# Optimization experiments

Hardware: AMD Instinct MI355X
Metric: run time of the kernel (lower is better)

## Reference

```python
import jax, jax.numpy as jnp
import numpy as np

B, N_P, N_S = 64, 50, 200
N_NODES = N_P * N_S          # 10000 nodes per graph (jobs x ops)
N_CAND = N_S + 1             # 201 candidates
INPUT_DIM, HIDDEN = 3, 64
NODE_DIM = 2 * HIDDEN        # h_nodes feature dim (=> actor in = 6*HIDDEN)
POOL_DIM = 4 * HIDDEN        # h_pooled dim (mean || max pooling)
H_ACTOR, H_CRITIC = 256, 256


def setup_inputs() -> dict:
    key = jax.random.key(0)
    ks = jax.random.split(key, 16)
    p = lambda k, sh: jax.random.normal(k, sh, jnp.float32) * 0.02
    x = jax.random.normal(ks[0], (B, N_NODES, INPUT_DIM), jnp.float32)
    candidate = jax.random.randint(ks[1], (B, N_CAND), 0, N_NODES)
    mask = jax.random.randint(ks[2], (B, N_CAND), 0, 2) > 0
    mask = mask.at[:, 0].set(True)  # guarantee at least one valid action per row
    return {
        "x": x, "candidate": candidate, "mask": mask,
        "fe_w1": p(ks[3], (INPUT_DIM, HIDDEN)), "fe_b1": jnp.zeros((HIDDEN,), jnp.float32),
        "fe_w2": p(ks[4], (HIDDEN, NODE_DIM)), "fe_b2": jnp.zeros((NODE_DIM,), jnp.float32),
        "a_w1": p(ks[5], (NODE_DIM + POOL_DIM, H_ACTOR)), "a_b1": jnp.zeros((H_ACTOR,), jnp.float32),
        "a_w2": p(ks[6], (H_ACTOR, H_ACTOR)), "a_b2": jnp.zeros((H_ACTOR,), jnp.float32),
        "a_w3": p(ks[7], (H_ACTOR, 1)), "a_b3": jnp.zeros((1,), jnp.float32),
        "c_w1": p(ks[8], (POOL_DIM, H_CRITIC)), "c_b1": jnp.zeros((H_CRITIC,), jnp.float32),
        "c_w2": p(ks[9], (H_CRITIC, H_CRITIC)), "c_b2": jnp.zeros((H_CRITIC,), jnp.float32),
        "c_w3": p(ks[10], (H_CRITIC, 1)), "c_b3": jnp.zeros((1,), jnp.float32),
    }


def _actor_critic(x, candidate, mask,
                  fe_w1, fe_b1, fe_w2, fe_b2,
                  a_w1, a_b1, a_w2, a_b2, a_w3, a_b3,
                  c_w1, c_b1, c_w2, c_b2, c_w3, c_b3):
    # --- feature_extract: per-node MLP embedding, graph-level pooling ---
    h = jax.nn.relu(jnp.einsum('bni,ih->bnh', x, fe_w1) + fe_b1)
    h_nodes = jax.nn.relu(jnp.einsum('bnh,hd->bnd', h, fe_w2) + fe_b2)   # [B, N, 2H]
    h_pooled = jnp.concatenate([h_nodes.mean(axis=1), h_nodes.max(axis=1)], axis=-1)  # [B, 4H]

    # --- gather candidate node features (torch.gather over node axis) ---
    cand_feat = jnp.take_along_axis(h_nodes, candidate[:, :, None], axis=1)  # [B, C, 2H]

    # --- concat broadcast pooled feature ---
    pooled_rep = jnp.broadcast_to(h_pooled[:, None, :], (cand_feat.shape[0], cand_feat.shape[1], h_pooled.shape[-1]))
    concat_fea = jnp.concatenate([cand_feat, pooled_rep], axis=-1)  # [B, C, 6H]

    # --- actor MLP (tanh hidden layers, linear out) ---
    a = jnp.tanh(concat_fea @ a_w1 + a_b1)
    a = jnp.tanh(a @ a_w2 + a_b2)
    scores = a @ a_w3 + a_b3                                    # [B, C, 1]

    # --- mask with -inf, softmax over candidate axis ---
    scores = jnp.where(mask[:, :, None], scores, -jnp.inf)
    pi = jax.nn.softmax(scores, axis=1)                          # [B, C, 1]

    # --- critic MLP on pooled feature ---
    c = jnp.tanh(h_pooled @ c_w1 + c_b1)
    c = jnp.tanh(c @ c_w2 + c_b2)
    v = c @ c_w3 + c_b3                                          # [B, 1]
    return pi, v


def reference(x, candidate, mask,
              fe_w1, fe_b1, fe_w2, fe_b2,
              a_w1, a_b1, a_w2, a_b2, a_w3, a_b3,
              c_w1, c_b1, c_w2, c_b2, c_w3, c_b3):
    return _actor_critic(x, candidate, mask,
                         fe_w1, fe_b1, fe_w2, fe_b2,
                         a_w1, a_b1, a_w2, a_b2, a_w3, a_b3,
                         c_w1, c_b1, c_w2, c_b2, c_w3, c_b3)
```

## Files before the change

### kernel.cpp

```cpp
#include <hip/hip_runtime.h>

#define NN 10000
#define NCAND 201
#define NB 64

typedef __attribute__((ext_vector_type(8))) short short8;
typedef __attribute__((ext_vector_type(4))) float f32x4;

__device__ __forceinline__ float bf2f(unsigned short u) {
  return __uint_as_float(((unsigned int)u) << 16);
}
__device__ __forceinline__ unsigned short f2bf(float f) {
  unsigned int u = __float_as_uint(f);
  u += 0x7FFFu + ((u >> 16) & 1u);
  return (unsigned short)(u >> 16);
}
__device__ __forceinline__ float fast_tanh(float x) {
  return 1.0f - 2.0f / (__expf(2.0f * x) + 1.0f);
}
__device__ __forceinline__ float gld(const void* p, long i, int f) {
  return f ? ((const float*)p)[i] : bf2f(((const unsigned short*)p)[i]);
}

__global__ __launch_bounds__(256)
void prep_kernel(const void* x, const void* w1, const void* b1, const void* w2,
                 const void* b2, const void* aw1, const void* ab1, const void* aw2,
                 const void* ab2, const void* aw3, const void* ab3,
                 const void* cw1, const void* cb1, const void* cw2, const void* cb2,
                 const void* cw3, const void* cb3,
                 const unsigned int* mask_w, const unsigned int* cand_w,
                 int* F, float* zero_base, int* scnt,
                 unsigned short* __restrict__ w2t, unsigned short* __restrict__ aw1t,
                 unsigned short* __restrict__ aw2t,
                 unsigned short* __restrict__ cw1t, unsigned short* __restrict__ cw2t) {
  const int t = threadIdx.x;
  const int j = blockIdx.x;

  if (j < 384) {
    __shared__ int cnts[5];
    if (t < 5) cnts[t] = 0;
    __syncthreads();
    const void* aps[5] = {w2, aw1, aw2, cw1, cw2};
#pragma unroll
    for (int a = 0; a < 5; ++a) {
      const unsigned short* p = (const unsigned short*)aps[a];
      if ((p[t] & 0x7F80u) >= 0x4300u) atomicAdd(&cnts[a], 1);
    }
    __syncthreads();
    const int Fw2 = cnts[0] > 32, Faw1 = cnts[1] > 32, Faw2 = cnts[2] > 32;
    const int Fcw1 = cnts[3] > 32, Fcw2 = cnts[4] > 32;
    int i = j * 256 + t;
    if (i < 128 * 64) { int n = i >> 6, k = i & 63; w2t[i] = f2bf(gld(w2, k * 128 + n, Fw2)); }
    if (i < 256 * 384) { int n = i / 384, k = i % 384; aw1t[i] = f2bf(gld(aw1, k * 256 + n, Faw1)); }
    if (i < 256 * 256) {
      int n = i >> 8, k = i & 255;
      aw2t[i] = f2bf(gld(aw2, k * 256 + n, Faw2));
      cw1t[i] = f2bf(gld(cw1, k * 256 + n, Fcw1));
      cw2t[i] = f2bf(gld(cw2, k * 256 + n, Fcw2));
    }
    return;
  }

  __shared__ int sh[3];
  if (t < 3) sh[t] = 0;
  __syncthreads();

  if (j < 401) {
    const void* ptrs[17] = {x, w1, b1, w2, b2, aw1, ab1, aw2, ab2, aw3, ab3,
                            cw1, cb1, cw2, cb2, cw3, cb3};
    const int sizes[17] = {1920000, 192, 64, 8192, 128, 98304, 256, 65536, 256,
                           256, 1, 65536, 256, 65536, 256, 256, 1};
    int a = j - 384;
    const unsigned short* p = (const unsigned short*)ptrs[a];
    int K = min(sizes[a], 2048);
    int c = 0;
    for (int i = t; i < K; i += 256)
      if ((p[i] & 0x7F80u) >= 0x4300u) c++;
    if (c) atomicAdd(&sh[0], c);
    __syncthreads();
    if (t == 0) F[a] = (sh[0] > (K >> 3)) ? 1 : 0;
  } else if (j == 401) {
    int flo = 0, fhi = 0, fgt = 0;
    for (int i = t; i < 3216; i += 256) {
      unsigned int w = mask_w[i];
      if ((w & 0xFFFFu) == 0x3F80u) flo = 1;
      if ((w >> 16) == 0x3F80u) fhi = 1;
      if (w > 1u) fgt = 1;
    }
    if (flo) sh[0] = 1;
    if (fhi) sh[1] = 1;
    if (fgt) sh[2] = 1;
    __syncthreads();
    if (t == 0) F[17] = sh[0] ? 2 : (sh[1] ? 3 : (sh[2] ? 1 : 0));
  } else if (j == 402) {
    int co = 0;
    for (int i = t; i < 1024; i += 256)
      if ((i & 1) && cand_w[i] != 0u) co = 1;
    if (co) sh[0] = 1;
    if (t < 64) scnt[t] = 0;
    __syncthreads();
    if (t == 0) F[18] = sh[0] ? 0 : 1;
  } else {
    zero_base[(j - 403) * 256 + t] = 0.f;
  }
}

__global__ __launch_bounds__(256, 4)
void fp_actorA_kernel(const void* __restrict__ x, const int* __restrict__ cand,
                      const void* __restrict__ w1, const void* __restrict__ b1,
                      const unsigned short* __restrict__ w2t,
                      const void* __restrict__ b2,
                      const int* __restrict__ F,
                      float* __restrict__ psum, float* __restrict__ pmax,
                      unsigned short* __restrict__ cfw) {
  __shared__ __align__(16) unsigned short pool[128 * 72];
  __shared__ float w1f[3 * 64];
  __shared__ float b1f[64];
  __shared__ float b2f[128];

  const int t = threadIdx.x;
  const int lane = t & 63;
  const int wv = t >> 6;
  const int F0 = F[0], F1 = F[1], F2 = F[2], F4 = F[4];

  if (blockIdx.x < 1024) {
    unsigned short* h1s = pool;
    const int b = blockIdx.x >> 4;
    const int s = blockIdx.x & 15;

    if (t < 192) w1f[t] = gld(w1, t, F1);
    if (t < 64) b1f[t] = gld(b1, t, F2);
    if (t < 128) b2f[t] = gld(b2, t, F4);

    short8 bfr[2][2];
#pragma unroll
    for (int nl = 0; nl < 2; ++nl)
#pragma unroll
      for (int ks = 0; ks < 2; ++ks) {
        int col = wv * 32 + nl * 16 + (lane & 15);
        bfr[nl][ks] = *(const short8*)(w2t + col * 64 + ((lane >> 4) * 8) + ks * 32);
      }
    __syncthreads();

    float csum[2] = {0.f, 0.f};
    float cmax[2] = {0.f, 0.f};
    const int m = t & 127;
    const int kg = t >> 7;

    float x0 = 0.f, x1 = 0.f, x2 = 0.f;
    if (s < 79) {
      int nb = s * 128;
      if (m < min(128, NN - nb)) {
        long xo = ((long)b * NN + nb + m) * 3;
        x0 = gld(x, xo, F0); x1 = gld(x, xo + 1, F0); x2 = gld(x, xo + 2, F0);
      }
    }

    for (int c = s; c < 79; c += 16) {
      int nb = c * 128;
      int cnt = (nb + 128 <= NN) ? 128 : (NN - nb);
      if (m < cnt) {
#pragma unroll
        for (int blk = 0; blk < 4; ++blk) {
          short8 v;
#pragma unroll
          for (int i = 0; i < 8; ++i) {
            int k = kg * 32 + blk * 8 + i;
            float vv = x0 * w1f[k] + x1 * w1f[64 + k] + x2 * w1f[128 + k] + b1f[k];
            v[i] = (short)f2bf(fmaxf(vv, 0.f));
          }
          *(short8*)(h1s + m * 72 + kg * 32 + blk * 8) = v;
        }
      }
      {
        int cn = c + 16;
        float nx0 = 0.f, nx1 = 0.f, nx2 = 0.f;
        if (cn < 79) {
          int nbn = cn * 128;
          if (m < min(128, NN - nbn)) {
            long xo = ((long)b * NN + nbn + m) * 3;
            nx0 = gld(x, xo, F0); nx1 = gld(x, xo + 1, F0); nx2 = gld(x, xo + 2, F0);
          }
        }
        __syncthreads();
        x0 = nx0; x1 = nx1; x2 = nx2;
      }
#pragma unroll
      for (int mt = 0; mt < 8; ++mt) {
        const unsigned short* ap = h1s + (mt * 16 + (lane & 15)) * 72 + ((lane >> 4) * 8);
        short8 af0 = *(const short8*)(ap);
        short8 af1 = *(const short8*)(ap + 32);
#pragma unroll
        for (int nl = 0; nl < 2; ++nl) {
          f32x4 acc = {0.f, 0.f, 0.f, 0.f};
          acc = __builtin_amdgcn_mfma_f32_16x16x32_bf16(af0, bfr[nl][0], acc, 0, 0, 0);
          acc = __builtin_amdgcn_mfma_f32_16x16x32_bf16(af1, bfr[nl][1], acc, 0, 0, 0);
          int col = wv * 32 + nl * 16 + (lane & 15);
          float bb = b2f[col];
#pragma unroll
          for (int r = 0; r < 4; ++r) {
            int row = mt * 16 + ((lane >> 4) * 4) + r;
            if (row < cnt) {
              float v = fmaxf(acc[r] + bb, 0.f);
              csum[nl] += v;
              cmax[nl] = fmaxf(cmax[nl], v);
            }
          }
        }
      }
      __syncthreads();
    }
#pragma unroll
    for (int nl = 0; nl < 2; ++nl) {
      csum[nl] += __shfl_xor(csum[nl], 16);
      csum[nl] += __shfl_xor(csum[nl], 32);
      cmax[nl] = fmaxf(cmax[nl], __shfl_xor(cmax[nl], 16));
      cmax[nl] = fmaxf(cmax[nl], __shfl_xor(cmax[nl], 32));
    }
    if (lane < 16) {
#pragma unroll
      for (int nl = 0; nl < 2; ++nl) {
        int col = wv * 32 + nl * 16 + lane;
        atomicAdd(&psum[b * 128 + col], csum[nl]);
        atomicMax((int*)&pmax[b * 128 + col], __float_as_int(cmax[nl]));
      }
    }
  } else {
    unsigned short* h1c = pool;
    unsigned short* cf = pool + 2560;
    const int idx = blockIdx.x - 1024;
    const int b = idx / 7;
    const int cb = idx % 7;
    const int cbase = cb * 29;
    const int C64 = F[18];

    if (t < 128) b2f[t] = gld(b2, t, F4);

    {
      int r = t & 31;
      int ci = cbase + r;
      if (ci > NCAND - 1) ci = NCAND - 1;
      long cidx = (long)b * NCAND + ci;
      int nd = C64 ? cand[2 * cidx] : cand[cidx];
      long xo = ((long)b * NN + nd) * 3;
      float x0 = gld(x, xo, F0), x1 = gld(x, xo + 1, F0), x2 = gld(x, xo + 2, F0);
      int kg = t >> 5;
#pragma unroll
      for (int i = 0; i < 8; ++i) {
        int k = kg * 8 + i;
        float v = x0 * gld(w1, k, F1) + x1 * gld(w1, 64 + k, F1) +
                  x2 * gld(w1, 128 + k, F1) + gld(b1, k, F2);
        h1c[r * 72 + k] = f2bf(fmaxf(v, 0.f));
      }
    }
    __syncthreads();

    {
      short8 af[2][2];
#pragma unroll
      for (int mt = 0; mt < 2; ++mt)
#pragma unroll
        for (int ks = 0; ks < 2; ++ks)
          af[mt][ks] = *(const short8*)(h1c + (mt * 16 + (lane & 15)) * 72 + ((lane >> 4) * 8) + ks * 32);
#pragma unroll
      for (int nl = 0; nl < 2; ++nl) {
        int col = wv * 32 + nl * 16 + (lane & 15);
        short8 bf0 = *(const short8*)(w2t + col * 64 + ((lane >> 4) * 8));
        short8 bf1 = *(const short8*)(w2t + col * 64 + ((lane >> 4) * 8) + 32);
        float bb = b2f[col];
#pragma unroll
        for (int mt = 0; mt < 2; ++mt) {
          f32x4 acc = {0.f, 0.f, 0.f, 0.f};
          acc = __builtin_amdgcn_mfma_f32_16x16x32_bf16(af[mt][0], bf0, acc, 0, 0, 0);
          acc = __builtin_amdgcn_mfma_f32_16x16x32_bf16(af[mt][1], bf1, acc, 0, 0, 0);
#pragma unroll
          for (int r = 0; r < 4; ++r) {
            int row = mt * 16 + ((lane >> 4) * 4) + r;
            cfw[(long)idx * 4096 + row * 128 + col] = f2bf(fmaxf(acc[r] + bb, 0.f));
          }
        }
      }
    }
  }
}

__global__ __launch_bounds__(256)
void pp_critic_kernel(const float* __restrict__ psum, const float* __restrict__ pmax,
                      const unsigned short* __restrict__ aw1t,
                      const void* __restrict__ ab1,
                      const unsigned short* __restrict__ cw1t,
                      const unsigned short* __restrict__ cw2t,
                      const void* __restrict__ cb1, const void* __restrict__ cb2,
                      const void* __restrict__ cw3, const void* __restrict__ cb3,
                      const int* __restrict__ F,
                      float* __restrict__ pact, void* __restrict__ out) {
  __shared__ float plf[256];
  __shared__ float c1f[256];
  __shared__ float red[4];
  const int t = threadIdx.x;
  const int b = blockIdx.x & 63;
  const int lane = t & 63, wv = t >> 6;

  if (blockIdx.x < 64) {
    const int F6 = F[6];
    if (t < 128) {
      plf[t] = bf2f(f2bf(psum[b * 128 + t] * (1.0f / 10000.0f)));
      plf[128 + t] = bf2f(f2bf(pmax[b * 128 + t]));
    }
    __syncthreads();
    float a = gld(ab1, t, F6);
    const unsigned short* row = aw1t + t * 384 + 128;
#pragma unroll
    for (int k8 = 0; k8 < 32; ++k8) {
      short8 w = *(const short8*)(row + k8 * 8);
#pragma unroll
      for (int j = 0; j < 8; ++j)
        a += plf[k8 * 8 + j] * bf2f((unsigned short)w[j]);
    }
    pact[b * 256 + t] = a;
  } else {
    const int OF = (F[0] + F[1] + F[3] + F[5] + F[7] + F[9] + F[11] + F[13] + F[15]) >= 5;
    const int F12 = F[12], F14 = F[14], F15 = F[15], F16 = F[16];
    if (t < 128) {
      plf[t] = psum[b * 128 + t] * (1.0f / 10000.0f);
      plf[128 + t] = pmax[b * 128 + t];
    }
    __syncthreads();
    {
      float a = gld(cb1, t, F12);
      const unsigned short* row = cw1t + t * 256;
#pragma unroll
      for (int k8 = 0; k8 < 32; ++k8) {
        short8 w = *(const short8*)(row + k8 * 8);
#pragma unroll
        for (int j = 0; j < 8; ++j)
          a += plf[k8 * 8 + j] * bf2f((unsigned short)w[j]);
      }
      c1f[t] = fast_tanh(a);
    }
    __syncthreads();
    {
      float a2 = gld(cb2, t, F14);
      const unsigned short* row = cw2t + t * 256;
#pragma unroll
      for (int k8 = 0; k8 < 32; ++k8) {
        short8 w = *(const short8*)(row + k8 * 8);
#pragma unroll
        for (int j = 0; j < 8; ++j)
          a2 += c1f[k8 * 8 + j] * bf2f((unsigned short)w[j]);
      }
      a2 = fast_tanh(a2);
      float p = a2 * gld(cw3, t, F15);
      for (int o = 32; o; o >>= 1) p += __shfl_xor(p, o);
      __syncthreads();
      if (lane == 0) red[wv] = p;
      __syncthreads();
      if (t == 0) {
        float v = red[0] + red[1] + red[2] + red[3] + gld(cb3, 0, F16);
        if (!(v == v)) v = 0.f;
        if (OF) ((float*)out)[NB * NCAND + b] = v;
        else ((unsigned short*)out)[NB * NCAND + b] = f2bf(v);
      }
    }
  }
}

__global__ __launch_bounds__(256)
void actorB_kernel(const unsigned short* __restrict__ cfw,
                   const void* __restrict__ ab2,
                   const void* __restrict__ aw3, const void* __restrict__ ab3,
                   const void* __restrict__ mask,
                   const int* __restrict__ F,
                   const float* __restrict__ pact,
                   const unsigned short* __restrict__ aw1t,
                   const unsigned short* __restrict__ aw2t,
                   float* __restrict__ scores, int* __restrict__ scnt,
                   void* __restrict__ out) {
  __shared__ __align__(16) unsigned short a1s[32 * 264];
  __shared__ __align__(16) unsigned short a2s[32 * 264];
  __shared__ float pactS[256], ab2f[256];
  __shared__ float red[4];
  __shared__ int amLast;

  const int t = threadIdx.x;
  const int b = blockIdx.x / 7;
  const int cb = blockIdx.x % 7;
  const int cbase = cb * 29;
  const int cntc = min(29, NCAND - cbase);
  const int lane = t & 63;
  const int wv = t >> 6;
  const int F8 = F[8], F9 = F[9], F10 = F[10];

  pactS[t] = pact[b * 256 + t];
  ab2f[t] = gld(ab2, t, F8);

  {
    f32x4 acc[2][4];
#pragma unroll
    for (int mt = 0; mt < 2; ++mt)
#pragma unroll
      for (int nt = 0; nt < 4; ++nt) acc[mt][nt] = (f32x4){0.f, 0.f, 0.f, 0.f};
    const unsigned short* cfb = cfw + (long)blockIdx.x * 4096;
#pragma unroll
    for (int ks = 0; ks < 4; ++ks) {
      short8 af0 = *(const short8*)(cfb + (lane & 15) * 128 + ks * 32 + ((lane >> 4) * 8));
      short8 af1 = *(const short8*)(cfb + (16 + (lane & 15)) * 128 + ks * 32 + ((lane >> 4) * 8));
#pragma unroll
      for (int nt = 0; nt < 4; ++nt) {
        int col = wv * 64 + nt * 16 + (lane & 15);
        short8 bfr = *(const short8*)(aw1t + col * 384 + ks * 32 + ((lane >> 4) * 8));
        acc[0][nt] = __builtin_amdgcn_mfma_f32_16x16x32_bf16(af0, bfr, acc[0][nt], 0, 0, 0);
        acc[1][nt] = __builtin_amdgcn_mfma_f32_16x16x32_bf16(af1, bfr, acc[1][nt], 0, 0, 0);
      }
    }
    __syncthreads();
#pragma unroll
    for (int mt = 0; mt < 2; ++mt)
#pragma unroll
      for (int nt = 0; nt < 4; ++nt) {
        int col = wv * 64 + nt * 16 + (lane & 15);
        float bb = pactS[col];
#pragma unroll
        for (int r = 0; r < 4; ++r) {
          int row = mt * 16 + ((lane >> 4) * 4) + r;
          a1s[row * 264 + col] = f2bf(fast_tanh(acc[mt][nt][r] + bb));
        }
      }
  }
  __syncthreads();

  {
    f32x4 acc[2][4];
#pragma unroll
    for (int mt = 0; mt < 2; ++mt)
#pragma unroll
      for (int nt = 0; nt < 4; ++nt) acc[mt][nt] = (f32x4){0.f, 0.f, 0.f, 0.f};
    for (int ks = 0; ks < 8; ++ks) {
      short8 af0 = *(const short8*)(a1s + (lane & 15) * 264 + ks * 32 + ((lane >> 4) * 8));
      short8 af1 = *(const short8*)(a1s + (16 + (lane & 15)) * 264 + ks * 32 + ((lane >> 4) * 8));
#pragma unroll
      for (int nt = 0; nt < 4; ++nt) {
        int col = wv * 64 + nt * 16 + (lane & 15);
        short8 bfr = *(const short8*)(aw2t + col * 256 + ks * 32 + ((lane >> 4) * 8));
        acc[0][nt] = __builtin_amdgcn_mfma_f32_16x16x32_bf16(af0, bfr, acc[0][nt], 0, 0, 0);
        acc[1][nt] = __builtin_amdgcn_mfma_f32_16x16x32_bf16(af1, bfr, acc[1][nt], 0, 0, 0);
      }
    }
#pragma unroll
    for (int mt = 0; mt < 2; ++mt)
#pragma unroll
      for (int nt = 0; nt < 4; ++nt) {
        int col = wv * 64 + nt * 16 + (lane & 15);
        float bb = ab2f[col];
#pragma unroll
        for (int r = 0; r < 4; ++r) {
          int row = mt * 16 + ((lane >> 4) * 4) + r;
          a2s[row * 264 + col] = f2bf(fast_tanh(acc[mt][nt][r] + bb));
        }
      }
  }
  __syncthreads();

  {
    int row = t >> 3, seg = t & 7;
    float p = 0.f;
#pragma unroll 8
    for (int i = 0; i < 32; ++i) {
      int k = seg * 32 + i;
      p += bf2f(a2s[row * 264 + k]) * gld(aw3, k, F9);
    }
    p += __shfl_xor(p, 1);
    p += __shfl_xor(p, 2);
    p += __shfl_xor(p, 4);
    if (seg == 0 && row < cntc)
      atomicExch(&scores[b * 256 + cbase + row], p + gld(ab3, 0, F10));
  }
  __syncthreads();

  if (t == 0) {
    __threadfence();
    amLast = (atomicAdd(&scnt[b], 1) == 6);
  }
  __syncthreads();
  if (!amLast) return;

  const int MM = F[17];
  const int OF = (F[0] + F[1] + F[3] + F[5] + F[7] + F[9] + F[11] + F[13] + F[15]) >= 5;
  float sraw = 0.f, sv = -1e30f;
  bool valid = false;
  if (t < NCAND) {
    sraw = atomicAdd(&scores[b * 256 + t], 0.0f);
    long idx = (long)b * NCAND + t;
    if (MM == 0)      valid = ((const int*)mask)[idx] != 0;
    else if (MM == 1) valid = ((const unsigned char*)mask)[idx] != 0;
    else if (MM == 2) valid = ((const unsigned short*)mask)[idx] != 0;
    else              valid = ((const unsigned int*)mask)[idx] != 0;
    if (valid) sv = sraw;
  }
  float m = sv;
  for (int o = 32; o; o >>= 1) m = fmaxf(m, __shfl_xor(m, o));
  if (lane == 0) red[wv] = m;
  __syncthreads();
  m = fmaxf(fmaxf(red[0], red[1]), fmaxf(red[2], red[3]));
  __syncthreads();
  float e = valid ? __expf(sraw - m) : 0.f;
  if (!(e == e)) e = 0.f;
  float ss = e;
  for (int o = 32; o; o >>= 1) ss += __shfl_xor(ss, o);
  if (lane == 0) red[wv] = ss;
  __syncthreads();
  float tot = red[0] + red[1] + red[2] + red[3];
  tot = fmaxf(tot, 1e-30f);
  if (t < NCAND) {
    float pv = e / tot;
    if (!(pv == pv)) pv = 0.f;
    if (OF) ((float*)out)[b * NCAND + t] = pv;
    else ((unsigned short*)out)[b * NCAND + t] = f2bf(pv);
  }
}

extern "C" void kernel_launch(void* const* d_in, const int* in_sizes, int n_in,
                              void* d_out, int out_size, void* d_ws, size_t ws_size,
                              hipStream_t stream) {
  const void* x = d_in[0];
  const int* cand = (const int*)d_in[1];
  const void* mask = d_in[2];
  const void* fe_w1 = d_in[3];
  const void* fe_b1 = d_in[4];
  const void* fe_w2 = d_in[5];
  const void* fe_b2 = d_in[6];
  const void* a_w1 = d_in[7];
  const void* a_b1 = d_in[8];
  const void* a_w2 = d_in[9];
  const void* a_b2 = d_in[10];
  const void* a_w3 = d_in[11];
  const void* a_b3 = d_in[12];
  const void* c_w1 = d_in[13];
  const void* c_b1 = d_in[14];
  const void* c_w2 = d_in[15];
  const void* c_b2 = d_in[16];
  const void* c_w3 = d_in[17];
  const void* c_b3 = d_in[18];

  char* ws = (char*)d_ws;
  float* psum = (float*)(ws + 0);
  float* pmax = (float*)(ws + 32768);
  float* scores = (float*)(ws + 65536);
  unsigned short* w2t = (unsigned short*)(ws + 131072);
  unsigned short* aw1t = (unsigned short*)(ws + 147456);
  unsigned short* aw2t = (unsigned short*)(ws + 344064);
  int* F = (int*)(ws + 475136);
  unsigned short* cw1t = (unsigned short*)(ws + 475264);
  unsigned short* cw2t = (unsigned short*)(ws + 606336);
  float* pact = (float*)(ws + 737408);
  unsigned short* cfw = (unsigned short*)(ws + 802944);
  int* scnt = (int*)(ws + 4472960);

  prep_kernel<<<467, 256, 0, stream>>>(x, fe_w1, fe_b1, fe_w2, fe_b2,
                                       a_w1, a_b1, a_w2, a_b2, a_w3, a_b3,
                                       c_w1, c_b1, c_w2, c_b2, c_w3, c_b3,
                                       (const unsigned int*)mask,
                                       (const unsigned int*)cand, F, psum, scnt,
                                       w2t, aw1t, aw2t, cw1t, cw2t);
  fp_actorA_kernel<<<1472, 256, 0, stream>>>(x, cand, fe_w1, fe_b1, w2t, fe_b2,
                                             F, psum, pmax, cfw);
  pp_critic_kernel<<<128, 256, 0, stream>>>(psum, pmax, aw1t, a_b1,
                                            cw1t, cw2t, c_b1, c_b2, c_w3, c_b3,
                                            F, pact, (void*)d_out);
  actorB_kernel<<<448, 256, 0, stream>>>(cfw, a_b2, a_w3, a_b3, mask, F, pact,
                                         aw1t, aw2t, scores, scnt, (void*)d_out);
}
```

Baseline: 164.9 us.

## Merge prep and feature-extract kernels; write per-slice pooling partials instead of atomics

The separate prep and feature-extraction kernels become one launch. Each feature block now re-detects the input dtype flags locally and reads fe_w2 directly instead of waiting for a transposed copy. Pooled sum and max go to per-slice partial buffers that the critic kernel reduces, which removes the global atomics and the zero-initialisation blocks. This saves a launch and its dependency barrier, at the cost of redundant flag detection and strided weight loads in every block.

```diff
diff --git a/kernel.cpp b/kernel.cpp
--- a/kernel.cpp
+++ b/kernel.cpp
@@ -22,35 +22,239 @@
   return f ? ((const float*)p)[i] : bf2f(((const unsigned short*)p)[i]);
 }
 
-__global__ __launch_bounds__(256)
-void prep_kernel(const void* x, const void* w1, const void* b1, const void* w2,
-                 const void* b2, const void* aw1, const void* ab1, const void* aw2,
-                 const void* ab2, const void* aw3, const void* ab3,
+__global__ __launch_bounds__(256, 4)
+void mega_kernel(const void* __restrict__ x, const int* __restrict__ cand,
+                 const void* w1, const void* b1, const void* w2, const void* b2,
+                 const void* aw1, const void* ab1, const void* aw2, const void* ab2,
+                 const void* aw3, const void* ab3,
                  const void* cw1, const void* cb1, const void* cw2, const void* cb2,
                  const void* cw3, const void* cb3,
                  const unsigned int* mask_w, const unsigned int* cand_w,
-                 int* F, float* zero_base, int* scnt,
-                 unsigned short* __restrict__ w2t, unsigned short* __restrict__ aw1t,
-                 unsigned short* __restrict__ aw2t,
+                 int* F, int* scnt,
+                 float* __restrict__ psumP, float* __restrict__ pmaxP,
+                 unsigned short* __restrict__ cfw,
+                 unsigned short* __restrict__ aw1t, unsigned short* __restrict__ aw2t,
                  unsigned short* __restrict__ cw1t, unsigned short* __restrict__ cw2t) {
+  __shared__ __align__(16) unsigned short pool[128 * 72];
+  __shared__ float w1f[3 * 64];
+  __shared__ float b1f[64];
+  __shared__ float b2f[128];
+  __shared__ int cnts[8];
+
   const int t = threadIdx.x;
   const int j = blockIdx.x;
-
-  if (j < 384) {
-    __shared__ int cnts[5];
-    if (t < 5) cnts[t] = 0;
-    __syncthreads();
-    const void* aps[5] = {w2, aw1, aw2, cw1, cw2};
-#pragma unroll
-    for (int a = 0; a < 5; ++a) {
-      const unsigned short* p = (const unsigned short*)aps[a];
-      if ((p[t] & 0x7F80u) >= 0x4300u) atomicAdd(&cnts[a], 1);
-    }
-    __syncthreads();
-    const int Fw2 = cnts[0] > 32, Faw1 = cnts[1] > 32, Faw2 = cnts[2] > 32;
-    const int Fcw1 = cnts[3] > 32, Fcw2 = cnts[4] > 32;
-    int i = j * 256 + t;
-    if (i < 128 * 64) { int n = i >> 6, k = i & 63; w2t[i] = f2bf(gld(w2, k * 128 + n, Fw2)); }
+  const int lane = t & 63;
+  const int wv = t >> 6;
+
+  if (j < 1472) {
+    if (t < 8) cnts[t] = 0;
+    __syncthreads();
+    {
+      if ((((const unsigned short*)x)[t] & 0x7F80u) >= 0x4300u) atomicAdd(&cnts[0], 1);
+      if (t < 192 && (((const unsigned short*)w1)[t] & 0x7F80u) >= 0x4300u) atomicAdd(&cnts[1], 1);
+      if (t < 64 && (((const unsigned short*)b1)[t] & 0x7F80u) >= 0x4300u) atomicAdd(&cnts[2], 1);
+      if (t < 128 && (((const unsigned short*)b2)[t] & 0x7F80u) >= 0x4300u) atomicAdd(&cnts[3], 1);
+      if ((((const unsigned short*)w2)[t] & 0x7F80u) >= 0x4300u) atomicAdd(&cnts[4], 1);
+      int co = 0;
+#pragma unroll
+      for (int q = 0; q < 4; ++q) {
+        int i = t * 4 + q;
+        if ((i & 1) && cand_w[i] != 0u) co = 1;
+      }
+      if (co) atomicAdd(&cnts[5], 1);
+    }
+    __syncthreads();
+    const int F0 = cnts[0] > 32, F1 = cnts[1] > 24, F2 = cnts[2] > 8;
+    const int F4 = cnts[3] > 16, Fw2 = cnts[4] > 32, C64 = cnts[5] == 0;
+
+    if (j < 1024) {
+      unsigned short* h1s = pool;
+      const int b = j >> 4;
+      const int s = j & 15;
+
+      if (t < 192) w1f[t] = gld(w1, t, F1);
+      if (t < 64) b1f[t] = gld(b1, t, F2);
+      if (t < 128) b2f[t] = gld(b2, t, F4);
+
+      short8 bfr[2][2];
+#pragma unroll
+      for (int nl = 0; nl < 2; ++nl)
+#pragma unroll
+        for (int ks = 0; ks < 2; ++ks) {
+          int col = wv * 32 + nl * 16 + (lane & 15);
+          short8 v;
+#pragma unroll
+          for (int jj = 0; jj < 8; ++jj) {
+            int k = (lane >> 4) * 8 + ks * 32 + jj;
+            v[jj] = (short)f2bf(gld(w2, (long)k * 128 + col, Fw2));
+          }
+          bfr[nl][ks] = v;
+        }
+      __syncthreads();
+
+      float csum[2] = {0.f, 0.f};
+      float cmax[2] = {0.f, 0.f};
+      const int m = t & 127;
+      const int kg = t >> 7;
+
+      float x0 = 0.f, x1 = 0.f, x2 = 0.f;
+      if (s < 79) {
+        int nb = s * 128;
+        if (m < min(128, NN - nb)) {
+          long xo = ((long)b * NN + nb + m) * 3;
+          x0 = gld(x, xo, F0); x1 = gld(x, xo + 1, F0); x2 = gld(x, xo + 2, F0);
+        }
+      }
+
+      for (int c = s; c < 79; c += 16) {
+        int nb = c * 128;
+        int cnt = (nb + 128 <= NN) ? 128 : (NN - nb);
+        if (m < cnt) {
+#pragma unroll
+          for (int blk = 0; blk < 4; ++blk) {
+            short8 v;
+#pragma unroll
+            for (int i = 0; i < 8; ++i) {
+              int k = kg * 32 + blk * 8 + i;
+              float vv = x0 * w1f[k] + x1 * w1f[64 + k] + x2 * w1f[128 + k] + b1f[k];
+              v[i] = (short)f2bf(fmaxf(vv, 0.f));
+            }
+            *(short8*)(h1s + m * 72 + kg * 32 + blk * 8) = v;
+          }
+        }
+        {
+          int cn = c + 16;
+          float nx0 = 0.f, nx1 = 0.f, nx2 = 0.f;
+          if (cn < 79) {
+            int nbn = cn * 128;
+            if (m < min(128, NN - nbn)) {
+              long xo = ((long)b * NN + nbn + m) * 3;
+              nx0 = gld(x, xo, F0); nx1 = gld(x, xo + 1, F0); nx2 = gld(x, xo + 2, F0);
+            }
+          }
+          __syncthreads();
+          x0 = nx0; x1 = nx1; x2 = nx2;
+        }
+#pragma unroll
+        for (int mt = 0; mt < 8; ++mt) {
+          const unsigned short* ap = h1s + (mt * 16 + (lane & 15)) * 72 + ((lane >> 4) * 8);
+          short8 af0 = *(const short8*)(ap);
+          short8 af1 = *(const short8*)(ap + 32);
+#pragma unroll
+          for (int nl = 0; nl < 2; ++nl) {
+            f32x4 acc = {0.f, 0.f, 0.f, 0.f};
+            acc = __builtin_amdgcn_mfma_f32_16x16x32_bf16(af0, bfr[nl][0], acc, 0, 0, 0);
+            acc = __builtin_amdgcn_mfma_f32_16x16x32_bf16(af1, bfr[nl][1], acc, 0, 0, 0);
+            int col = wv * 32 + nl * 16 + (lane & 15);
+            float bb = b2f[col];
+#pragma unroll
+            for (int r = 0; r < 4; ++r) {
+              int row = mt * 16 + ((lane >> 4) * 4) + r;
+              if (row < cnt) {
+                float v = fmaxf(acc[r] + bb, 0.f);
+                csum[nl] += v;
+                cmax[nl] = fmaxf(cmax[nl], v);
+              }
+            }
+          }
+        }
+        __syncthreads();
+      }
+#pragma unroll
+      for (int nl = 0; nl < 2; ++nl) {
+        csum[nl] += __shfl_xor(csum[nl], 16);
+        csum[nl] += __shfl_xor(csum[nl], 32);
+        cmax[nl] = fmaxf(cmax[nl], __shfl_xor(cmax[nl], 16));
+        cmax[nl] = fmaxf(cmax[nl], __shfl_xor(cmax[nl], 32));
+      }
+      if (lane < 16) {
+#pragma unroll
+        for (int nl = 0; nl < 2; ++nl) {
+          int col = wv * 32 + nl * 16 + lane;
+          psumP[((long)b * 16 + s) * 128 + col] = csum[nl];
+          pmaxP[((long)b * 16 + s) * 128 + col] = cmax[nl];
+        }
+      }
+    } else {
+      unsigned short* h1c = pool;
+      unsigned short* cf = pool + 2560;
+      const int idx = j - 1024;
+      const int b = idx / 7;
+      const int cb = idx % 7;
+      const int cbase = cb * 29;
+
+      if (t < 128) b2f[t] = gld(b2, t, F4);
+
+      {
+        int r = t & 31;
+        int ci = cbase + r;
+        if (ci > NCAND - 1) ci = NCAND - 1;
+        long cidx = (long)b * NCAND + ci;
+        int nd = C64 ? cand[2 * cidx] : cand[cidx];
+        long xo = ((long)b * NN + nd) * 3;
+        float x0 = gld(x, xo, F0), x1 = gld(x, xo + 1, F0), x2 = gld(x, xo + 2, F0);
+        int kg = t >> 5;
+#pragma unroll
+        for (int i = 0; i < 8; ++i) {
+          int k = kg * 8 + i;
+          float v = x0 * gld(w1, k, F1) + x1 * gld(w1, 64 + k, F1) +
+                    x2 * gld(w1, 128 + k, F1) + gld(b1, k, F2);
+          h1c[r * 72 + k] = f2bf(fmaxf(v, 0.f));
+        }
+      }
+      __syncthreads();
+
+      {
+        short8 af[2][2];
+#pragma unroll
+        for (int mt = 0; mt < 2; ++mt)
+#pragma unroll
+          for (int ks = 0; ks < 2; ++ks)
+            af[mt][ks] = *(const short8*)(h1c + (mt * 16 + (lane & 15)) * 72 + ((lane >> 4) * 8) + ks * 32);
+#pragma unroll
+        for (int nl = 0; nl < 2; ++nl) {
+          int col = wv * 32 + nl * 16 + (lane & 15);
+          short8 bf0, bf1;
+#pragma unroll
+          for (int jj = 0; jj < 8; ++jj) {
+            int k = (lane >> 4) * 8 + jj;
+            bf0[jj] = (short)f2bf(gld(w2, (long)k * 128 + col, Fw2));
+            bf1[jj] = (short)f2bf(gld(w2, (long)(k + 32) * 128 + col, Fw2));
+          }
+          float bb = b2f[col];
+#pragma unroll
+          for (int mt = 0; mt < 2; ++mt) {
+            f32x4 acc = {0.f, 0.f, 0.f, 0.f};
+            acc = __builtin_amdgcn_mfma_f32_16x16x32_bf16(af[mt][0], bf0, acc, 0, 0, 0);
+            acc = __builtin_amdgcn_mfma_f32_16x16x32_bf16(af[mt][1], bf1, acc, 0, 0, 0);
+#pragma unroll
+            for (int r = 0; r < 4; ++r) {
+              int row = mt * 16 + ((lane >> 4) * 4) + r;
+              cfw[(long)idx * 4096 + row * 128 + col] = f2bf(fmaxf(acc[r] + bb, 0.f));
+            }
+          }
+        }
+      }
+    }
+    return;
+  }
+
+  if (t < 8) cnts[t] = 0;
+  __syncthreads();
+
+  if (j < 1856) {
+    const unsigned short* pa = (const unsigned short*)aw1;
+    const unsigned short* pb = (const unsigned short*)aw2;
+    const unsigned short* pc = (const unsigned short*)cw1;
+    const unsigned short* pd = (const unsigned short*)cw2;
+    if ((pa[t] & 0x7F80u) >= 0x4300u) atomicAdd(&cnts[0], 1);
+    if ((pb[t] & 0x7F80u) >= 0x4300u) atomicAdd(&cnts[1], 1);
+    if ((pc[t] & 0x7F80u) >= 0x4300u) atomicAdd(&cnts[2], 1);
+    if ((pd[t] & 0x7F80u) >= 0x4300u) atomicAdd(&cnts[3], 1);
+    __syncthreads();
+    const int Faw1 = cnts[0] > 32, Faw2 = cnts[1] > 32;
+    const int Fcw1 = cnts[2] > 32, Fcw2 = cnts[3] > 32;
+    int i = (j - 1472) * 256 + t;
     if (i < 256 * 384) { int n = i / 384, k = i % 384; aw1t[i] = f2bf(gld(aw1, k * 256 + n, Faw1)); }
     if (i < 256 * 256) {
       int n = i >> 8, k = i & 255;
@@ -58,28 +262,21 @@
       cw1t[i] = f2bf(gld(cw1, k * 256 + n, Fcw1));
       cw2t[i] = f2bf(gld(cw2, k * 256 + n, Fcw2));
     }
-    return;
-  }
-
-  __shared__ int sh[3];
-  if (t < 3) sh[t] = 0;
-  __syncthreads();
-
-  if (j < 401) {
+  } else if (j < 1873) {
     const void* ptrs[17] = {x, w1, b1, w2, b2, aw1, ab1, aw2, ab2, aw3, ab3,
                             cw1, cb1, cw2, cb2, cw3, cb3};
     const int sizes[17] = {1920000, 192, 64, 8192, 128, 98304, 256, 65536, 256,
                            256, 1, 65536, 256, 65536, 256, 256, 1};
-    int a = j - 384;
+    int a = j - 1856;
     const unsigned short* p = (const unsigned short*)ptrs[a];
     int K = min(sizes[a], 2048);
     int c = 0;
     for (int i = t; i < K; i += 256)
       if ((p[i] & 0x7F80u) >= 0x4300u) c++;
-    if (c) atomicAdd(&sh[0], c);
-    __syncthreads();
-    if (t == 0) F[a] = (sh[0] > (K >> 3)) ? 1 : 0;
-  } else if (j == 401) {
+    if (c) atomicAdd(&cnts[0], c);
+    __syncthreads();
+    if (t == 0) F[a] = (cnts[0] > (K >> 3)) ? 1 : 0;
+  } else if (j == 1873) {
     int flo = 0, fhi = 0, fgt = 0;
     for (int i = t; i < 3216; i += 256) {
       unsigned int w = mask_w[i];
@@ -87,205 +284,24 @@
       if ((w >> 16) == 0x3F80u) fhi = 1;
       if (w > 1u) fgt = 1;
     }
-    if (flo) sh[0] = 1;
-    if (fhi) sh[1] = 1;
-    if (fgt) sh[2] = 1;
-    __syncthreads();
-    if (t == 0) F[17] = sh[0] ? 2 : (sh[1] ? 3 : (sh[2] ? 1 : 0));
-  } else if (j == 402) {
+    if (flo) cnts[0] = 1;
+    if (fhi) cnts[1] = 1;
+    if (fgt) cnts[2] = 1;
+    __syncthreads();
+    if (t == 0) F[17] = cnts[0] ? 2 : (cnts[1] ? 3 : (cnts[2] ? 1 : 0));
+  } else {
     int co = 0;
     for (int i = t; i < 1024; i += 256)
       if ((i & 1) && cand_w[i] != 0u) co = 1;
-    if (co) sh[0] = 1;
+    if (co) cnts[0] = 1;
     if (t < 64) scnt[t] = 0;
     __syncthreads();
-    if (t == 0) F[18] = sh[0] ? 0 : 1;
-  } else {
-    zero_base[(j - 403) * 256 + t] = 0.f;
-  }
-}
-
-__global__ __launch_bounds__(256, 4)
-void fp_actorA_kernel(const void* __restrict__ x, const int* __restrict__ cand,
-                      const void* __restrict__ w1, const void* __restrict__ b1,
-                      const unsigned short* __restrict__ w2t,
-                      const void* __restrict__ b2,
-                      const int* __restrict__ F,
-                      float* __restrict__ psum, float* __restrict__ pmax,
-                      unsigned short* __restrict__ cfw) {
-  __shared__ __align__(16) unsigned short pool[128 * 72];
-  __shared__ float w1f[3 * 64];
-  __shared__ float b1f[64];
-  __shared__ float b2f[128];
-
-  const int t = threadIdx.x;
-  const int lane = t & 63;
-  const int wv = t >> 6;
-  const int F0 = F[0], F1 = F[1], F2 = F[2], F4 = F[4];
-
-  if (blockIdx.x < 1024) {
-    unsigned short* h1s = pool;
-    const int b = blockIdx.x >> 4;
-    const int s = blockIdx.x & 15;
-
-    if (t < 192) w1f[t] = gld(w1, t, F1);
-    if (t < 64) b1f[t] = gld(b1, t, F2);
-    if (t < 128) b2f[t] = gld(b2, t, F4);
-
-    short8 bfr[2][2];
-#pragma unroll
-    for (int nl = 0; nl < 2; ++nl)
-#pragma unroll
-      for (int ks = 0; ks < 2; ++ks) {
-        int col = wv * 32 + nl * 16 + (lane & 15);
-        bfr[nl][ks] = *(const short8*)(w2t + col * 64 + ((lane >> 4) * 8) + ks * 32);
-      }
-    __syncthreads();
-
-    float csum[2] = {0.f, 0.f};
-    float cmax[2] = {0.f, 0.f};
-    const int m = t & 127;
-    const int kg = t >> 7;
-
-    float x0 = 0.f, x1 = 0.f, x2 = 0.f;
-    if (s < 79) {
-      int nb = s * 128;
-      if (m < min(128, NN - nb)) {
-        long xo = ((long)b * NN + nb + m) * 3;
-        x0 = gld(x, xo, F0); x1 = gld(x, xo + 1, F0); x2 = gld(x, xo + 2, F0);
-      }
-    }
-
-    for (int c = s; c < 79; c += 16) {
-      int nb = c * 128;
-      int cnt = (nb + 128 <= NN) ? 128 : (NN - nb);
-      if (m < cnt) {
-#pragma unroll
-        for (int blk = 0; blk < 4; ++blk) {
-          short8 v;
-#pragma unroll
-          for (int i = 0; i < 8; ++i) {
-            int k = kg * 32 + blk * 8 + i;
-            float vv = x0 * w1f[k] + x1 * w1f[64 + k] + x2 * w1f[128 + k] + b1f[k];
-            v[i] = (short)f2bf(fmaxf(vv, 0.f));
-          }
-          *(short8*)(h1s + m * 72 + kg * 32 + blk * 8) = v;
-        }
-      }
-      {
-        int cn = c + 16;
-        float nx0 = 0.f, nx1 = 0.f, nx2 = 0.f;
-        if (cn < 79) {
-          int nbn = cn * 128;
-          if (m < min(128, NN - nbn)) {
-            long xo = ((long)b * NN + nbn + m) * 3;
-            nx0 = gld(x, xo, F0); nx1 = gld(x, xo + 1, F0); nx2 = gld(x, xo + 2, F0);
-          }
-        }
-        __syncthreads();
-        x0 = nx0; x1 = nx1; x2 = nx2;
-      }
-#pragma unroll
-      for (int mt = 0; mt < 8; ++mt) {
-        const unsigned short* ap = h1s + (mt * 16 + (lane & 15)) * 72 + ((lane >> 4) * 8);
-        short8 af0 = *(const short8*)(ap);
-        short8 af1 = *(const short8*)(ap + 32);
-#pragma unroll
-        for (int nl = 0; nl < 2; ++nl) {
-          f32x4 acc = {0.f, 0.f, 0.f, 0.f};
-          acc = __builtin_amdgcn_mfma_f32_16x16x32_bf16(af0, bfr[nl][0], acc, 0, 0, 0);
-          acc = __builtin_amdgcn_mfma_f32_16x16x32_bf16(af1, bfr[nl][1], acc, 0, 0, 0);
-          int col = wv * 32 + nl * 16 + (lane & 15);
-          float bb = b2f[col];
-#pragma unroll
-          for (int r = 0; r < 4; ++r) {
-            int row = mt * 16 + ((lane >> 4) * 4) + r;
-            if (row < cnt) {
-              float v = fmaxf(acc[r] + bb, 0.f);
-              csum[nl] += v;
-              cmax[nl] = fmaxf(cmax[nl], v);
-            }
-          }
-        }
-      }
-      __syncthreads();
-    }
-#pragma unroll
-    for (int nl = 0; nl < 2; ++nl) {
-      csum[nl] += __shfl_xor(csum[nl], 16);
-      csum[nl] += __shfl_xor(csum[nl], 32);
-      cmax[nl] = fmaxf(cmax[nl], __shfl_xor(cmax[nl], 16));
-      cmax[nl] = fmaxf(cmax[nl], __shfl_xor(cmax[nl], 32));
-    }
-    if (lane < 16) {
-#pragma unroll
-      for (int nl = 0; nl < 2; ++nl) {
-        int col = wv * 32 + nl * 16 + lane;
-        atomicAdd(&psum[b * 128 + col], csum[nl]);
-        atomicMax((int*)&pmax[b * 128 + col], __float_as_int(cmax[nl]));
-      }
-    }
-  } else {
-    unsigned short* h1c = pool;
-    unsigned short* cf = pool + 2560;
-    const int idx = blockIdx.x - 1024;
-    const int b = idx / 7;
-    const int cb = idx % 7;
-    const int cbase = cb * 29;
-    const int C64 = F[18];
-
-    if (t < 128) b2f[t] = gld(b2, t, F4);
-
-    {
-      int r = t & 31;
-      int ci = cbase + r;
-      if (ci > NCAND - 1) ci = NCAND - 1;
-      long cidx = (long)b * NCAND + ci;
-      int nd = C64 ? cand[2 * cidx] : cand[cidx];
-      long xo = ((long)b * NN + nd) * 3;
-      float x0 = gld(x, xo, F0), x1 = gld(x, xo + 1, F0), x2 = gld(x, xo + 2, F0);
-      int kg = t >> 5;
-#pragma unroll
-      for (int i = 0; i < 8; ++i) {
-        int k = kg * 8 + i;
-        float v = x0 * gld(w1, k, F1) + x1 * gld(w1, 64 + k, F1) +
-                  x2 * gld(w1, 128 + k, F1) + gld(b1, k, F2);
-        h1c[r * 72 + k] = f2bf(fmaxf(v, 0.f));
-      }
-    }
-    __syncthreads();
-
-    {
-      short8 af[2][2];
-#pragma unroll
-      for (int mt = 0; mt < 2; ++mt)
-#pragma unroll
-        for (int ks = 0; ks < 2; ++ks)
-          af[mt][ks] = *(const short8*)(h1c + (mt * 16 + (lane & 15)) * 72 + ((lane >> 4) * 8) + ks * 32);
-#pragma unroll
-      for (int nl = 0; nl < 2; ++nl) {
-        int col = wv * 32 + nl * 16 + (lane & 15);
-        short8 bf0 = *(const short8*)(w2t + col * 64 + ((lane >> 4) * 8));
-        short8 bf1 = *(const short8*)(w2t + col * 64 + ((lane >> 4) * 8) + 32);
-        float bb = b2f[col];
-#pragma unroll
-        for (int mt = 0; mt < 2; ++mt) {
-          f32x4 acc = {0.f, 0.f, 0.f, 0.f};
-          acc = __builtin_amdgcn_mfma_f32_16x16x32_bf16(af[mt][0], bf0, acc, 0, 0, 0);
-          acc = __builtin_amdgcn_mfma_f32_16x16x32_bf16(af[mt][1], bf1, acc, 0, 0, 0);
-#pragma unroll
-          for (int r = 0; r < 4; ++r) {
-            int row = mt * 16 + ((lane >> 4) * 4) + r;
-            cfw[(long)idx * 4096 + row * 128 + col] = f2bf(fmaxf(acc[r] + bb, 0.f));
-          }
-        }
-      }
-    }
+    if (t == 0) F[18] = cnts[0] ? 0 : 1;
   }
 }
 
 __global__ __launch_bounds__(256)
-void pp_critic_kernel(const float* __restrict__ psum, const float* __restrict__ pmax,
+void pp_critic_kernel(const float* __restrict__ psumP, const float* __restrict__ pmaxP,
                       const unsigned short* __restrict__ aw1t,
                       const void* __restrict__ ab1,
                       const unsigned short* __restrict__ cw1t,
@@ -301,11 +317,20 @@
   const int b = blockIdx.x & 63;
   const int lane = t & 63, wv = t >> 6;
 
+  float ssum = 0.f, smax = 0.f;
+  if (t < 128) {
+#pragma unroll
+    for (int sl = 0; sl < 16; ++sl) {
+      ssum += psumP[((long)b * 16 + sl) * 128 + t];
+      smax = fmaxf(smax, pmaxP[((long)b * 16 + sl) * 128 + t]);
+    }
+  }
+
   if (blockIdx.x < 64) {
     const int F6 = F[6];
     if (t < 128) {
-      plf[t] = bf2f(f2bf(psum[b * 128 + t] * (1.0f / 10000.0f)));
-      plf[128 + t] = bf2f(f2bf(pmax[b * 128 + t]));
+      plf[t] = bf2f(f2bf(ssum * (1.0f / 10000.0f)));
+      plf[128 + t] = bf2f(f2bf(smax));
     }
     __syncthreads();
     float a = gld(ab1, t, F6);
@@ -322,8 +347,8 @@
     const int OF = (F[0] + F[1] + F[3] + F[5] + F[7] + F[9] + F[11] + F[13] + F[15]) >= 5;
     const int F12 = F[12], F14 = F[14], F15 = F[15], F16 = F[16];
     if (t < 128) {
-      plf[t] = psum[b * 128 + t] * (1.0f / 10000.0f);
-      plf[128 + t] = pmax[b * 128 + t];
+      plf[t] = ssum * (1.0f / 10000.0f);
+      plf[128 + t] = smax;
     }
     __syncthreads();
     {
@@ -543,10 +568,7 @@
   const void* c_b3 = d_in[18];
 
   char* ws = (char*)d_ws;
-  float* psum = (float*)(ws + 0);
-  float* pmax = (float*)(ws + 32768);
   float* scores = (float*)(ws + 65536);
-  unsigned short* w2t = (unsigned short*)(ws + 131072);
   unsigned short* aw1t = (unsigned short*)(ws + 147456);
   unsigned short* aw2t = (unsigned short*)(ws + 344064);
   int* F = (int*)(ws + 475136);
@@ -555,16 +577,16 @@
   float* pact = (float*)(ws + 737408);
   unsigned short* cfw = (unsigned short*)(ws + 802944);
   int* scnt = (int*)(ws + 4472960);
-
-  prep_kernel<<<467, 256, 0, stream>>>(x, fe_w1, fe_b1, fe_w2, fe_b2,
-                                       a_w1, a_b1, a_w2, a_b2, a_w3, a_b3,
-                                       c_w1, c_b1, c_w2, c_b2, c_w3, c_b3,
-                                       (const unsigned int*)mask,
-                                       (const unsigned int*)cand, F, psum, scnt,
-                                       w2t, aw1t, aw2t, cw1t, cw2t);
-  fp_actorA_kernel<<<1472, 256, 0, stream>>>(x, cand, fe_w1, fe_b1, w2t, fe_b2,
-                                             F, psum, pmax, cfw);
-  pp_critic_kernel<<<128, 256, 0, stream>>>(psum, pmax, aw1t, a_b1,
+  float* psumP = (float*)(ws + 4473216);
+  float* pmaxP = (float*)(ws + 4997504);
+
+  mega_kernel<<<1875, 256, 0, stream>>>(x, cand, fe_w1, fe_b1, fe_w2, fe_b2,
+                                        a_w1, a_b1, a_w2, a_b2, a_w3, a_b3,
+                                        c_w1, c_b1, c_w2, c_b2, c_w3, c_b3,
+                                        (const unsigned int*)mask,
+                                        (const unsigned int*)cand, F, scnt,
+                                        psumP, pmaxP, cfw, aw1t, aw2t, cw1t, cw2t);
+  pp_critic_kernel<<<128, 256, 0, stream>>>(psumP, pmaxP, aw1t, a_b1,
                                             cw1t, cw2t, c_b1, c_b2, c_w3, c_b3,
                                             F, pact, (void*)d_out);
   actorB_kernel<<<448, 256, 0, stream>>>(cfw, a_b2, a_w3, a_b3, mask, F, pact,
```

Result: no change. 161.9 us (-1.8%).
